# Optimization experiments

Measured on AMD Instinct MI355X. Metric: run time of the kernel, lower is better.

## Reference

```python
import math
import jax, jax.numpy as jnp
import numpy as np

D = 192      # d_model
NH = 8       # heads
NL = 2       # levels
NP = 4       # points
HD = D // NH # head dim = 24
GROUPS = 32


def layer_norm(x, g, b, eps=1e-5):
    mu = x.mean(-1, keepdims=True)
    var = ((x - mu) ** 2).mean(-1, keepdims=True)
    return (x - mu) / jnp.sqrt(var + eps) * g + b


def group_norm(x, g, b, eps=1e-5):
    # x: [B, C, H, W]
    B, C, H, W = x.shape
    xg = x.reshape(B, GROUPS, C // GROUPS, H, W)
    mu = xg.mean((2, 3, 4), keepdims=True)
    var = ((xg - mu) ** 2).mean((2, 3, 4), keepdims=True)
    xn = ((xg - mu) / jnp.sqrt(var + eps)).reshape(B, C, H, W)
    return xn * g[None, :, None, None] + b[None, :, None, None]


def pos_embed_2d(H, W):
    # PositionalEncoding2D(96, normalize=True) with an all-valid mask
    eps = 1e-6
    scale = 2 * math.pi
    npf = 96
    y = (jnp.arange(1, H + 1, dtype=jnp.float32) - 0.5) / (H + eps) * scale
    x = (jnp.arange(1, W + 1, dtype=jnp.float32) - 0.5) / (W + eps) * scale
    dim_t = 10000.0 ** (2.0 * (jnp.arange(npf) // 2).astype(jnp.float32) / npf)
    def enc(v):
        p = v[:, None] / dim_t  # [N, 96]
        return jnp.stack([jnp.sin(p[:, 0::2]), jnp.cos(p[:, 1::2])], -1).reshape(v.shape[0], npf)
    pe_y, pe_x = enc(y), enc(x)
    pos = jnp.concatenate([
        jnp.broadcast_to(pe_y[:, None, :], (H, W, npf)),
        jnp.broadcast_to(pe_x[None, :, :], (H, W, npf)),
    ], -1)  # [H, W, 192] (y-part first, like torch cat((pos_y, pos_x)))
    return pos.reshape(H * W, 2 * npf)


def ms_sample(value_h, loc, H, W):
    # value_h: [B, NH, H*W, HD]; loc: [B, NH, Lq, NP, 2] normalized to [0,1]
    # Replicates F.grid_sample(mode='bilinear', padding_mode='zeros', align_corners=False)
    B, _, Lq, P, _ = loc.shape
    x = loc[..., 0] * W - 0.5
    y = loc[..., 1] * H - 0.5
    x0 = jnp.floor(x)
    y0 = jnp.floor(y)
    wx = x - x0
    wy = y - y0
    def corner(xc, yc, w):
        valid = (xc >= 0) & (xc <= W - 1) & (yc >= 0) & (yc <= H - 1)
        xi = jnp.clip(xc, 0, W - 1).astype(jnp.int32)
        yi = jnp.clip(yc, 0, H - 1).astype(jnp.int32)
        idx = (yi * W + xi).reshape(B, NH, Lq * P)
        g = jnp.take_along_axis(value_h, idx[..., None], axis=2).reshape(B, NH, Lq, P, HD)
        return g * (w * valid)[..., None]
    return (corner(x0, y0, (1 - wx) * (1 - wy))
            + corner(x0 + 1, y0, wx * (1 - wy))
            + corner(x0, y0 + 1, (1 - wx) * wy)
            + corner(x0 + 1, y0 + 1, wx * wy))


def encoder_forward(src, pos, ref_pts, shapes, p):
    B, L, _ = src.shape
    starts = np.cumsum([0] + [h * w for h, w in shapes])
    offset_norm = jnp.array([[w, h] for h, w in shapes], jnp.float32)  # [NL, 2] = (W, H)
    out = src
    n_layers = p['so_W'].shape[0]
    for i in range(n_layers):
        q = out + pos
        off = (q @ p['so_W'][i] + p['so_b'][i]).reshape(B, L, NH, NL, NP, 2)
        aw = (q @ p['aw_W'][i] + p['aw_b'][i]).reshape(B, L, NH, NL * NP)
        aw = jax.nn.softmax(aw, -1).reshape(B, L, NH, NL, NP)
        loc = ref_pts[None, :, None, :, None, :] + off / offset_norm[None, None, None, :, None, :]
        v = (out @ p['vp_W'][i] + p['vp_b'][i]).reshape(B, L, NH, HD).transpose(0, 2, 1, 3)
        sampled = []
        for l, (h, w) in enumerate(shapes):
            vl = v[:, :, starts[l]:starts[l + 1], :]
            locl = loc[:, :, :, l].transpose(0, 2, 1, 3, 4)  # [B, NH, L, NP, 2]
            sampled.append(ms_sample(vl, locl, h, w))
        sampled = jnp.stack(sampled, 3)  # [B, NH, L, NL, NP, HD]
        awh = aw.transpose(0, 2, 1, 3, 4)  # [B, NH, L, NL, NP]
        attn = jnp.einsum('bhqlp,bhqlpc->bhqc', awh, sampled)
        attn = attn.transpose(0, 2, 1, 3).reshape(B, L, D)
        attn = attn @ p['op_W'][i] + p['op_b'][i]
        out = layer_norm(out + attn, p['ln1_g'][i], p['ln1_b'][i])
        ff = jax.nn.relu(out @ p['l1_W'][i] + p['l1_b'][i]) @ p['l2_W'][i] + p['l2_b'][i]
        out = layer_norm(out + ff, p['ln2_g'][i], p['ln2_b'][i])
    return out


def _feature_encoder(feat0, feat1, proj_w0, proj_b0, gn_g0, gn_b0,
                     proj_w1, proj_b1, gn_g1, gn_b1, level_embed, p):
    feats = [feat0, feat1]
    projs = [(proj_w0, proj_b0, gn_g0, gn_b0), (proj_w1, proj_b1, gn_g1, gn_b1)]
    shapes = [(int(f.shape[2]), int(f.shape[3])) for f in feats]
    B = feat0.shape[0]
    srcs, poss, refs = [], [], []
    for l, f in enumerate(feats):
        w, b, g, bb = projs[l]
        s = jnp.einsum('bchw,oc->bohw', f, w) + b[None, :, None, None]  # 1x1 conv
        s = group_norm(s, g, bb)
        srcs.append(s.reshape(B, D, -1).transpose(0, 2, 1))
        poss.append(pos_embed_2d(*shapes[l]) + level_embed[l])
        h, wdt = shapes[l]
        ry, rx = jnp.meshgrid(jnp.linspace(0.5, h - 0.5, h) / h,
                              jnp.linspace(0.5, wdt - 0.5, wdt) / wdt, indexing='ij')
        refs.append(jnp.stack([rx.reshape(-1), ry.reshape(-1)], -1))
    src = jnp.concatenate(srcs, 1)                # [B, Ltot, D]
    pos = jnp.concatenate(poss, 0)[None]          # [1, Ltot, D]
    # full-size images => masks all False => valid_ratios == 1
    ref_pts = jnp.broadcast_to(jnp.concatenate(refs, 0)[:, None, :], (src.shape[1], NL, 2))
    mem = encoder_forward(src, pos, ref_pts, shapes, p)
    n0 = shapes[0][0] * shapes[0][1]
    m0 = mem[:, :n0].reshape(B, shapes[0][0], shapes[0][1], D).transpose(0, 3, 1, 2)
    m1 = mem[:, n0:].reshape(B, shapes[1][0], shapes[1][1], D).transpose(0, 3, 1, 2)
    return m0, m1


def setup_inputs() -> dict:
    key = jax.random.key(0)
    ks = jax.random.split(key, 20)
    L = 6
    s = 0.02
    d = {}
    d['feat0'] = jax.random.normal(ks[0], (2, D, 96, 96), jnp.float32)
    d['feat1'] = jax.random.normal(ks[1], (2, D, 48, 48), jnp.float32)
    d['imgs'] = jax.random.normal(ks[2], (2, 3, 384, 384), jnp.float32)
    d['proj_w0'] = jax.random.normal(ks[3], (D, D), jnp.float32) * s
    d['proj_b0'] = jnp.zeros((D,), jnp.float32)
    d['gn_g0'] = jnp.ones((D,), jnp.float32)
    d['gn_b0'] = jnp.zeros((D,), jnp.float32)
    d['proj_w1'] = jax.random.normal(ks[4], (D, D), jnp.float32) * s
    d['proj_b1'] = jnp.zeros((D,), jnp.float32)
    d['gn_g1'] = jnp.ones((D,), jnp.float32)
    d['gn_b1'] = jnp.zeros((D,), jnp.float32)
    d['level_embed'] = jax.random.normal(ks[5], (NL, D), jnp.float32) * s
    d['so_W'] = jax.random.normal(ks[6], (L, D, NH * NL * NP * 2), jnp.float32) * s
    d['so_b'] = jax.random.normal(ks[7], (L, NH * NL * NP * 2), jnp.float32) * s
    d['aw_W'] = jax.random.normal(ks[8], (L, D, NH * NL * NP), jnp.float32) * s
    d['aw_b'] = jnp.zeros((L, NH * NL * NP), jnp.float32)
    d['vp_W'] = jax.random.normal(ks[9], (L, D, D), jnp.float32) * s
    d['vp_b'] = jnp.zeros((L, D), jnp.float32)
    d['op_W'] = jax.random.normal(ks[10], (L, D, D), jnp.float32) * s
    d['op_b'] = jnp.zeros((L, D), jnp.float32)
    d['ln1_g'] = jnp.ones((L, D), jnp.float32)
    d['ln1_b'] = jnp.zeros((L, D), jnp.float32)
    d['l1_W'] = jax.random.normal(ks[11], (L, D, 256), jnp.float32) * s
    d['l1_b'] = jnp.zeros((L, 256), jnp.float32)
    d['l2_W'] = jax.random.normal(ks[12], (L, 256, D), jnp.float32) * s
    d['l2_b'] = jnp.zeros((L, D), jnp.float32)
    d['ln2_g'] = jnp.ones((L, D), jnp.float32)
    d['ln2_b'] = jnp.zeros((L, D), jnp.float32)
    return d


def reference(feat0, feat1, imgs, proj_w0, proj_b0, gn_g0, gn_b0,
              proj_w1, proj_b1, gn_g1, gn_b1, level_embed,
              so_W, so_b, aw_W, aw_b, vp_W, vp_b, op_W, op_b,
              ln1_g, ln1_b, l1_W, l1_b, l2_W, l2_b, ln2_g, ln2_b):
    # imgs is only used for image sizes; full-size => all-valid masks
    p = dict(so_W=so_W, so_b=so_b, aw_W=aw_W, aw_b=aw_b, vp_W=vp_W, vp_b=vp_b,
             op_W=op_W, op_b=op_b, ln1_g=ln1_g, ln1_b=ln1_b,
             l1_W=l1_W, l1_b=l1_b, l2_W=l2_W, l2_b=l2_b, ln2_g=ln2_g, ln2_b=ln2_b)
    return _feature_encoder(feat0, feat1, proj_w0, proj_b0, gn_g0, gn_b0,
                            proj_w1, proj_b1, gn_g1, gn_b1, level_embed, p)
```

## Files before the change

kernel.cpp:

```cpp
#include <hip/hip_runtime.h>
#include <hip/hip_bf16.h>
#include <math.h>

#define Bb 2
#define Dm 192
#define NHh 8
#define HDd 24
#define N0 9216
#define N1 2304
#define LSEQ 11520
#define FFD 256
#define Mrows (Bb*LSEQ)

typedef __attribute__((ext_vector_type(8))) short short8;
typedef __attribute__((ext_vector_type(4))) float f32x4;

#define F_OUT 0
#define F_PRE (F_OUT + 4423680)
#define F_POS (F_PRE + 4423680)
#define F_LOC (F_POS + 2211840)
#define F_AW  (F_LOC + 2949120)
#define F_QB  (F_AW + 1474560)
#define F_OB  (F_QB + 2211840)
#define F_AH  (F_OB + 2211840)
#define F_WT16 (F_AH + 2949120)
#define F_BC  (F_WT16 + 626688)
#define F_GNS (F_BC + 1152)
#define F_V2  (F_GNS + 256)

#define WL_STRIDE 208896
#define WL_SOAW 0
#define WL_VP   36864
#define WL_OP   73728
#define WL_L1   110592
#define WL_L2   159744

__device__ inline __hip_bfloat16 f2b(float f) { return __float2bfloat16(f); }
__device__ inline unsigned short f2bu(float f) {
    __hip_bfloat16 h = __float2bfloat16(f);
    return *reinterpret_cast<unsigned short*>(&h);
}

__global__ void k_pos(float* pos, const float* level_embed) {
    int idx = blockIdx.x * 256 + threadIdx.x;
    if (idx >= LSEQ * Dm) return;
    int t = idx / Dm, d = idx % Dm;
    int lvl, row, col, H, W;
    if (t < N0) { lvl = 0; H = 96; W = 96; row = t / 96; col = t % 96; }
    else        { lvl = 1; H = 48; W = 48; int tl = t - N0; row = tl / 48; col = tl % 48; }
    int k = d % 96;
    float v;
    if (d < 96) v = (row + 0.5f) / ((float)H + 1e-6f) * 6.2831853071795864f;
    else        v = (col + 0.5f) / ((float)W + 1e-6f) * 6.2831853071795864f;
    float expo = (float)(k - (k & 1)) / 96.0f;
    float tm = exp2f(expo * 13.287712379549449f);
    float p = v / tm;
    float pe = (k & 1) ? cosf(p) : sinf(p);
    pos[idx] = pe + level_embed[lvl * Dm + d];
}

__global__ void k_prep(const float* soW, const float* awW, const float* vpW,
        const float* opW, const float* l1W, const float* l2W,
        const float* sob, const float* awb,
        __hip_bfloat16* WT, float* BC) {
    int idx = blockIdx.x * 256 + threadIdx.x;
    if (idx < 6 * 192) {
        int i = idx / 192, n = idx % 192;
        BC[idx] = (n < 128) ? sob[i * 128 + n] : awb[i * 64 + (n - 128)];
    }
    if (idx >= 6 * WL_STRIDE) return;
    int i = idx / WL_STRIDE; int r = idx % WL_STRIDE;
    float v;
    if (r < 36864)       { int n = r / 192, k = r % 192;
        v = (n < 128) ? soW[((size_t)i * 192 + k) * 128 + n]
                      : awW[((size_t)i * 192 + k) * 64 + (n - 128)]; }
    else if (r < 73728)  { int q = r - 36864;  int n = q / 192, k = q % 192;
        v = vpW[((size_t)i * 192 + k) * 192 + n]; }
    else if (r < 110592) { int q = r - 73728;  int n = q / 192, k = q % 192;
        v = opW[((size_t)i * 192 + k) * 192 + n]; }
    else if (r < 159744) { int q = r - 110592; int n = q / 192, k = q % 192;
        v = l1W[((size_t)i * 192 + k) * 256 + n]; }
    else                 { int q = r - 159744; int n = q / 256, k = q % 256;
        v = l2W[((size_t)i * 256 + k) * 192 + n]; }
    WT[idx] = f2b(v);
}

__global__ void k_prepc(const float* w0, const float* w1, __hip_bfloat16* cwb) {
    int idx = blockIdx.x * 256 + threadIdx.x;
    if (idx >= 2 * 36864) return;
    const float* w = (idx < 36864) ? w0 : w1;
    int r = idx % 36864;
    cwb[idx] = f2b(w[r]);
}

__global__ void k_tf(const float* feat, __hip_bfloat16* out, int HW, int st) {
    __shared__ float tile[32][33];
    int t0 = blockIdx.x * 32, c0 = blockIdx.y * 32, b = blockIdx.z;
    int tx = threadIdx.x, ty = threadIdx.y;
    #pragma unroll
    for (int k = 0; k < 4; k++) {
        int c = c0 + ty + k * 8;
        tile[ty + k * 8][tx] = feat[((size_t)b * Dm + c) * HW + t0 + tx];
    }
    __syncthreads();
    #pragma unroll
    for (int k = 0; k < 4; k++) {
        int t = t0 + ty + k * 8;
        out[((size_t)b * LSEQ + st + t) * Dm + c0 + tx] = f2b(tile[tx][ty + k * 8]);
    }
}

__global__ __launch_bounds__(192) void k_gnp(const float* __restrict__ pre,
        float* __restrict__ part) {
    int bid = blockIdx.x;
    int b = bid / 120; int r = bid % 120;
    int l = (r >= 96) ? 1 : 0; int ch = l ? (r - 96) : r;
    int start = b * LSEQ + (l ? N0 : 0) + ch * 96;
    int d = threadIdx.x;
    float s = 0.f, sq = 0.f;
    for (int t = 0; t < 96; t++) {
        float x = pre[(size_t)(start + t) * Dm + d];
        s += x; sq += x * x;
    }
    __shared__ float ls[192], lq[192];
    ls[d] = s; lq[d] = sq;
    __syncthreads();
    if (d < 32) {
        float a = 0.f, b2 = 0.f;
        #pragma unroll
        for (int j = 0; j < 6; j++) { a += ls[d * 6 + j]; b2 += lq[d * 6 + j]; }
        part[((size_t)bid * 32 + d) * 2]     = a;
        part[((size_t)bid * 32 + d) * 2 + 1] = b2;
    }
}

__global__ void k_gnf(const float* __restrict__ part, float* __restrict__ gns) {
    int bid = blockIdx.x;
    int b = bid >> 6; int l = (bid >> 5) & 1; int g = bid & 31;
    int nch = l ? 24 : 96;
    int base = b * 120 + (l ? 96 : 0);
    int tid = threadIdx.x;
    float s = 0.f, q = 0.f;
    for (int c = tid; c < nch; c += 64) {
        s += part[((size_t)(base + c) * 32 + g) * 2];
        q += part[((size_t)(base + c) * 32 + g) * 2 + 1];
    }
    for (int m = 1; m < 64; m <<= 1) { s += __shfl_xor(s, m, 64); q += __shfl_xor(q, m, 64); }
    if (tid == 0) {
        float total = (float)((l ? N1 : N0) * 6);
        float mean = s / total;
        float var = q / total - mean * mean;
        gns[bid * 2] = mean;
        gns[bid * 2 + 1] = rsqrtf(var + 1e-5f);
    }
}

__global__ void k_gnnorm(const float* srcp, const float* gns,
        const float* g0, const float* b0, const float* g1, const float* b1,
        const float* pos, float* out, __hip_bfloat16* ob, __hip_bfloat16* qb) {
    int idx = blockIdx.x * 256 + threadIdx.x;
    if (idx >= Bb * LSEQ * Dm) return;
    int d = idx % Dm;
    int t = (idx / Dm) % LSEQ;
    int l = (t < N0) ? 0 : 1;
    int g = d / 6;
    int b = idx / (Dm * LSEQ);
    int sid = ((b * 2 + l) * 32 + g) * 2;
    float mean = gns[sid], rstd = gns[sid + 1];
    float gg = l ? g1[d] : g0[d];
    float bbv = l ? b1[d] : b0[d];
    float v = (srcp[idx] - mean) * rstd * gg + bbv;
    out[idx] = v;
    ob[idx] = f2b(v);
    qb[idx] = f2b(v + pos[idx - (size_t)b * LSEQ * Dm]);
}

template<int KSTEPS>
__global__ __launch_bounds__(256) void k_gemm(
        const __hip_bfloat16* __restrict__ A,
        const __hip_bfloat16* __restrict__ Bt,
        const float* __restrict__ bias,
        float* __restrict__ Cf, int N) {
    constexpr int K = KSTEPS * 32;
    int wid = threadIdx.x >> 6, lane = threadIdx.x & 63;
    int lg = lane >> 4, lr = lane & 15;
    int row0 = blockIdx.x * 64 + wid * 16;
    int col0 = blockIdx.y * 64;
    const short* a_base = (const short*)A + (size_t)(row0 + lr) * K + lg * 8;
    const short* b_base = (const short*)Bt + (size_t)(col0 + lr) * K + lg * 8;
    f32x4 acc[4] = {};
    #pragma unroll
    for (int kk = 0; kk < KSTEPS; kk++) {
        short8 af = *(const short8*)(a_base + kk * 32);
        #pragma unroll
        for (int n = 0; n < 4; n++) {
            short8 bfr = *(const short8*)(b_base + (size_t)n * 16 * K + kk * 32);
            acc[n] = __builtin_amdgcn_mfma_f32_16x16x32_bf16(af, bfr, acc[n], 0, 0, 0);
        }
    }
    #pragma unroll
    for (int n = 0; n < 4; n++) {
        int col = col0 + n * 16 + lr;
        float bv = bias[col];
        #pragma unroll
        for (int r = 0; r < 4; r++) {
            int row = row0 + lg * 4 + r;
            Cf[(size_t)row * N + col] = acc[n][r] + bv;
        }
    }
}

__global__ __launch_bounds__(192) void k_soawvp(
        const __hip_bfloat16* __restrict__ QB,
        const __hip_bfloat16* __restrict__ OB,
        const __hip_bfloat16* __restrict__ BtS,
        const __hip_bfloat16* __restrict__ BtV,
        const float* __restrict__ biasS,
        const float* __restrict__ biasV,
        float* __restrict__ LOC, float* __restrict__ AW,
        float* __restrict__ VF) {
    constexpr int K = 192;
    int wid = threadIdx.x >> 6, lane = threadIdx.x & 63;
    int lg = lane >> 4, lr = lane & 15;
    int row0 = blockIdx.x * 32;
    int col0 = wid * 64;
    int role = blockIdx.y;
    const short* A  = (const short*)(role ? OB : QB);
    const short* Bt = (const short*)(role ? BtV : BtS);
    const float* bias = role ? biasV : biasS;
    short8 bw[24];
    {
        const short* b_base = Bt + (size_t)(col0 + lr) * K + lg * 8;
        #pragma unroll
        for (int n = 0; n < 4; n++)
            #pragma unroll
            for (int kk = 0; kk < 6; kk++)
                bw[n * 6 + kk] = *(const short8*)(b_base + (size_t)n * 16 * K + kk * 32);
    }
    #pragma unroll
    for (int rg = 0; rg < 2; rg++) {
        const short* a_base = A + (size_t)(row0 + rg * 16 + lr) * K + lg * 8;
        f32x4 acc[4] = {};
        #pragma unroll
        for (int kk = 0; kk < 6; kk++) {
            short8 af = *(const short8*)(a_base + kk * 32);
            #pragma unroll
            for (int n = 0; n < 4; n++)
                acc[n] = __builtin_amdgcn_mfma_f32_16x16x32_bf16(af, bw[n * 6 + kk], acc[n], 0, 0, 0);
        }
        #pragma unroll
        for (int n = 0; n < 4; n++) {
            float bv = bias[col0 + n * 16 + lr];
            #pragma unroll
            for (int r = 0; r < 4; r++) acc[n][r] += bv;
        }
        int rbase = row0 + rg * 16;
        if (role) {
            #pragma unroll
            for (int n = 0; n < 4; n++) {
                int col = col0 + n * 16 + lr;
                #pragma unroll
                for (int r = 0; r < 4; r++)
                    VF[(size_t)(rbase + lg * 4 + r) * Dm + col] = acc[n][r];
            }
        } else if (wid == 2) {
            #pragma unroll
            for (int n = 0; n < 4; n++) {
                #pragma unroll
                for (int r = 0; r < 4; r++) {
                    float v = acc[n][r];
                    float m = v;
                    m = fmaxf(m, __shfl_xor(m, 1)); m = fmaxf(m, __shfl_xor(m, 2));
                    m = fmaxf(m, __shfl_xor(m, 4));
                    float e = expf(v - m);
                    float sm = e;
                    sm += __shfl_xor(sm, 1); sm += __shfl_xor(sm, 2); sm += __shfl_xor(sm, 4);
                    AW[(size_t)(rbase + lg * 4 + r) * 64 + n * 16 + lr] = e / sm;
                }
            }
        } else {
            #pragma unroll
            for (int r = 0; r < 4; r++) {
                int row = rbase + lg * 4 + r;
                int t = (row >= LSEQ) ? row - LSEQ : row;
                int rr, cc, Ht, Wt;
                if (t < N0) { Ht = 96; Wt = 96; rr = t / 96; cc = t % 96; }
                else        { Ht = 48; Wt = 48; int tl = t - N0; rr = tl / 48; cc = tl % 48; }
                float refx = (cc + 0.5f) / (float)Wt;
                float refy = (rr + 0.5f) / (float)Ht;
                #pragma unroll
                for (int n = 0; n < 4; n++) {
                    int col = col0 + n * 16 + lr;
                    int j = col >> 1, comp = col & 1;
                    float sc = (j & 4) ? 48.f : 96.f;
                    LOC[(size_t)row * 128 + col] = (comp ? refy : refx) + acc[n][r] / sc;
                }
            }
        }
    }
}

template<bool LAST>
__global__ __launch_bounds__(256) void k_tail(
        const float* __restrict__ Vin,
        float* __restrict__ LOC, float* __restrict__ AW,
        const __hip_bfloat16* __restrict__ BtOp, const float* __restrict__ bOp,
        const __hip_bfloat16* __restrict__ Bt1, const float* __restrict__ b1,
        const __hip_bfloat16* __restrict__ Bt2, const float* __restrict__ b2,
        const float* __restrict__ g1, const float* __restrict__ t1,
        const float* __restrict__ g2, const float* __restrict__ t2,
        const float* __restrict__ pos,
        float* __restrict__ OUTp,
        const __hip_bfloat16* __restrict__ BtS,
        const __hip_bfloat16* __restrict__ BtV,
        const float* __restrict__ biasS, const float* __restrict__ biasV,
        float* __restrict__ Vout) {
    __shared__ __align__(16) short ybf[32][200];
    __shared__ __align__(16) short hid[32][264];
    __shared__ float aw_s[32][64];
    __shared__ float ps[4][32], pq[4][32];
    int tid = threadIdx.x;
    int wid = tid >> 6, lane = tid & 63, lg = lane >> 4, lr = lane & 15;
    int row0 = blockIdx.x * 32;
    float yres[2][3][4];
    {
        float* loc_s = (float*)&hid[0][0];
        for (int idx = tid; idx < 32 * 128; idx += 256)
            loc_s[idx] = LOC[(size_t)row0 * 128 + idx];
        for (int idx = tid; idx < 32 * 64; idx += 256)
            aw_s[idx >> 6][idx & 63] = AW[(size_t)row0 * 64 + idx];
        __syncthreads();
        for (int tt6 = 0; tt6 < 6; tt6++) {
            int id = tid + tt6 * 256;
            int tl = id / 48;
            int l48 = id - tl * 48;
            int h = l48 / 6, dq = l48 - h * 6;
            int row = row0 + tl;
            int bb = (row >= LSEQ) ? 1 : 0;
            const float* vbase = Vin + (size_t)bb * LSEQ * Dm + h * HDd + dq * 4;
            float a0 = 0.f, a1 = 0.f, a2 = 0.f, a3 = 0.f;
            #pragma unroll
            for (int lp = 0; lp < 8; lp++) {
                int l = lp >> 2;
                int Wl = l ? 48 : 96, Hl = l ? 48 : 96, st = l ? N0 : 0;
                float a  = aw_s[tl][h * 8 + lp];
                float lx = loc_s[tl * 128 + (h * 8 + lp) * 2];
                float ly = loc_s[tl * 128 + (h * 8 + lp) * 2 + 1];
                float x = lx * (float)Wl - 0.5f, y = ly * (float)Hl - 0.5f;
                float x0f = floorf(x), y0f = floorf(y);
                float wx = x - x0f, wy = y - y0f;
                int x0 = (int)x0f, y0 = (int)y0f;
                #pragma unroll
                for (int cy = 0; cy < 2; cy++) {
                    int yi = y0 + cy;
                    float wyv = cy ? wy : 1.f - wy;
                    bool vy = (yi >= 0) && (yi < Hl);
                    int yc = min(max(yi, 0), Hl - 1);
                    #pragma unroll
                    for (int cx = 0; cx < 2; cx++) {
                        int xi = x0 + cx;
                        float wv = (cx ? wx : 1.f - wx) * wyv;
                        bool ok = vy && (xi >= 0) && (xi < Wl);
                        int xc = min(max(xi, 0), Wl - 1);
                        float cw = ok ? a * wv : 0.f;
                        float4 g4 = *(const float4*)(vbase + (size_t)(st + yc * Wl + xc) * Dm);
                        a0 += cw * g4.x; a1 += cw * g4.y;
                        a2 += cw * g4.z; a3 += cw * g4.w;
                    }
                }
            }
            ushort4 o4;
            o4.x = f2bu(a0); o4.y = f2bu(a1); o4.z = f2bu(a2); o4.w = f2bu(a3);
            *(ushort4*)&ybf[tl][h * HDd + dq * 4] = o4;
        }
        __syncthreads();
    }
    {
        float resid[2][3][4];
        #pragma unroll
        for (int rg = 0; rg < 2; rg++)
            #pragma unroll
            for (int n = 0; n < 3; n++) {
                int col = wid * 48 + n * 16 + lr;
                #pragma unroll
                for (int r = 0; r < 4; r++)
                    resid[rg][n][r] = OUTp[(size_t)(row0 + rg * 16 + lg * 4 + r) * Dm + col];
            }
        const short* b_base = (const short*)BtOp + (size_t)(wid * 48 + lr) * 192 + lg * 8;
        f32x4 acc[2][3] = {};
        #pragma unroll
        for (int kk = 0; kk < 6; kk++) {
            short8 af0 = *(const short8*)&ybf[lr][lg * 8 + kk * 32];
            short8 af1 = *(const short8*)&ybf[16 + lr][lg * 8 + kk * 32];
            #pragma unroll
            for (int n = 0; n < 3; n++) {
                short8 bfr = *(const short8*)(b_base + (size_t)n * 16 * 192 + kk * 32);
                acc[0][n] = __builtin_amdgcn_mfma_f32_16x16x32_bf16(af0, bfr, acc[0][n], 0, 0, 0);
                acc[1][n] = __builtin_amdgcn_mfma_f32_16x16x32_bf16(af1, bfr, acc[1][n], 0, 0, 0);
            }
        }
        #pragma unroll
        for (int rg = 0; rg < 2; rg++) {
            float s[4] = {0.f, 0.f, 0.f, 0.f}, q[4] = {0.f, 0.f, 0.f, 0.f};
            #pragma unroll
            for (int n = 0; n < 3; n++) {
                int col = wid * 48 + n * 16 + lr;
                float bv = bOp[col];
                #pragma unroll
                for (int r = 0; r < 4; r++) {
                    float v = acc[rg][n][r] + bv + resid[rg][n][r];
                    acc[rg][n][r] = v;
                    s[r] += v; q[r] += v * v;
                }
            }
            #pragma unroll
            for (int r = 0; r < 4; r++) {
                #pragma unroll
                for (int m = 1; m < 16; m <<= 1) {
                    s[r] += __shfl_xor(s[r], m); q[r] += __shfl_xor(q[r], m);
                }
            }
            if (lr == 0) {
                #pragma unroll
                for (int r = 0; r < 4; r++) {
                    ps[wid][rg * 16 + lg * 4 + r] = s[r];
                    pq[wid][rg * 16 + lg * 4 + r] = q[r];
                }
            }
        }
        __syncthreads();
        #pragma unroll
        for (int rg = 0; rg < 2; rg++) {
            float mean[4], rstd[4];
            #pragma unroll
            for (int r = 0; r < 4; r++) {
                int rl = rg * 16 + lg * 4 + r;
                float S = ps[0][rl] + ps[1][rl] + ps[2][rl] + ps[3][rl];
                float Q = pq[0][rl] + pq[1][rl] + pq[2][rl] + pq[3][rl];
                mean[r] = S * (1.f / Dm);
                float var = Q * (1.f / Dm) - mean[r] * mean[r];
                rstd[r] = rsqrtf(var + 1e-5f);
            }
            #pragma unroll
            for (int n = 0; n < 3; n++) {
                int col = wid * 48 + n * 16 + lr;
                float gg = g1[col], bb = t1[col];
                #pragma unroll
                for (int r = 0; r < 4; r++) {
                    float y = (acc[rg][n][r] - mean[r]) * rstd[r] * gg + bb;
                    yres[rg][n][r] = y;
                    ybf[rg * 16 + lg * 4 + r][col] = (short)f2bu(y);
                }
            }
        }
        __syncthreads();
    }
    {
        const short* b_base = (const short*)Bt1 + (size_t)(wid * 64 + lr) * 192 + lg * 8;
        f32x4 acc[2][4] = {};
        #pragma unroll
        for (int kk = 0; kk < 6; kk++) {
            short8 af0 = *(const short8*)&ybf[lr][lg * 8 + kk * 32];
            short8 af1 = *(const short8*)&ybf[16 + lr][lg * 8 + kk * 32];
            #pragma unroll
            for (int n = 0; n < 4; n++) {
                short8 bfr = *(const short8*)(b_base + (size_t)n * 16 * 192 + kk * 32);
                acc[0][n] = __builtin_amdgcn_mfma_f32_16x16x32_bf16(af0, bfr, acc[0][n], 0, 0, 0);
                acc[1][n] = __builtin_amdgcn_mfma_f32_16x16x32_bf16(af1, bfr, acc[1][n], 0, 0, 0);
            }
        }
        #pragma unroll
        for (int rg = 0; rg < 2; rg++)
            #pragma unroll
            for (int n = 0; n < 4; n++) {
                int col = wid * 64 + n * 16 + lr;
                float bv = b1[col];
                #pragma unroll
                for (int r = 0; r < 4; r++)
                    hid[rg * 16 + lg * 4 + r][col] = (short)f2bu(fmaxf(acc[rg][n][r] + bv, 0.f));
            }
        __syncthreads();
    }
    {
        const short* b_base = (const short*)Bt2 + (size_t)(wid * 48 + lr) * 256 + lg * 8;
        f32x4 acc[2][3] = {};
        #pragma unroll
        for (int kk = 0; kk < 8; kk++) {
            short8 af0 = *(const short8*)&hid[lr][lg * 8 + kk * 32];
            short8 af1 = *(const short8*)&hid[16 + lr][lg * 8 + kk * 32];
            #pragma unroll
            for (int n = 0; n < 3; n++) {
                short8 bfr = *(const short8*)(b_base + (size_t)n * 16 * 256 + kk * 32);
                acc[0][n] = __builtin_amdgcn_mfma_f32_16x16x32_bf16(af0, bfr, acc[0][n], 0, 0, 0);
                acc[1][n] = __builtin_amdgcn_mfma_f32_16x16x32_bf16(af1, bfr, acc[1][n], 0, 0, 0);
            }
        }
        #pragma unroll
        for (int rg = 0; rg < 2; rg++) {
            float s[4] = {0.f, 0.f, 0.f, 0.f}, q[4] = {0.f, 0.f, 0.f, 0.f};
            #pragma unroll
            for (int n = 0; n < 3; n++) {
                int col = wid * 48 + n * 16 + lr;
                float bv = b2[col];
                #pragma unroll
                for (int r = 0; r < 4; r++) {
                    float v = acc[rg][n][r] + bv + yres[rg][n][r];
                    acc[rg][n][r] = v;
                    s[r] += v; q[r] += v * v;
                }
            }
            #pragma unroll
            for (int r = 0; r < 4; r++) {
                #pragma unroll
                for (int m = 1; m < 16; m <<= 1) {
                    s[r] += __shfl_xor(s[r], m); q[r] += __shfl_xor(q[r], m);
                }
            }
            if (lr == 0) {
                #pragma unroll
                for (int r = 0; r < 4; r++) {
                    ps[wid][rg * 16 + lg * 4 + r] = s[r];
                    pq[wid][rg * 16 + lg * 4 + r] = q[r];
                }
            }
        }
        __syncthreads();
        #pragma unroll
        for (int rg = 0; rg < 2; rg++) {
            float mean[4], rstd[4];
            #pragma unroll
            for (int r = 0; r < 4; r++) {
                int rl = rg * 16 + lg * 4 + r;
                float S = ps[0][rl] + ps[1][rl] + ps[2][rl] + ps[3][rl];
                float Q = pq[0][rl] + pq[1][rl] + pq[2][rl] + pq[3][rl];
                mean[r] = S * (1.f / Dm);
                float var = Q * (1.f / Dm) - mean[r] * mean[r];
                rstd[r] = rsqrtf(var + 1e-5f);
            }
            #pragma unroll
            for (int n = 0; n < 3; n++) {
                int col = wid * 48 + n * 16 + lr;
                float gg = g2[col], bb = t2[col];
                #pragma unroll
                for (int r = 0; r < 4; r++) {
                    int row = row0 + rg * 16 + lg * 4 + r;
                    int rl = rg * 16 + lg * 4 + r;
                    float y = (acc[rg][n][r] - mean[r]) * rstd[r] * gg + bb;
                    OUTp[(size_t)row * Dm + col] = y;
                    if (!LAST) {
                        ybf[rl][col] = (short)f2bu(y);
                        int tp = (row >= LSEQ) ? row - LSEQ : row;
                        hid[rl][col] = (short)f2bu(y + pos[(size_t)tp * Dm + col]);
                    }
                }
            }
        }
    }
    if (LAST) return;
    __syncthreads();
    {
        const short* b_base = (const short*)BtV + (size_t)(wid * 48 + lr) * 192 + lg * 8;
        f32x4 acc[2][3] = {};
        #pragma unroll
        for (int kk = 0; kk < 6; kk++) {
            short8 af0 = *(const short8*)&ybf[lr][lg * 8 + kk * 32];
            short8 af1 = *(const short8*)&ybf[16 + lr][lg * 8 + kk * 32];
            #pragma unroll
            for (int n = 0; n < 3; n++) {
                short8 bfr = *(const short8*)(b_base + (size_t)n * 16 * 192 + kk * 32);
                acc[0][n] = __builtin_amdgcn_mfma_f32_16x16x32_bf16(af0, bfr, acc[0][n], 0, 0, 0);
                acc[1][n] = __builtin_amdgcn_mfma_f32_16x16x32_bf16(af1, bfr, acc[1][n], 0, 0, 0);
            }
        }
        #pragma unroll
        for (int rg = 0; rg < 2; rg++)
            #pragma unroll
            for (int n = 0; n < 3; n++) {
                int col = wid * 48 + n * 16 + lr;
                float bv = biasV[col];
                #pragma unroll
                for (int r = 0; r < 4; r++)
                    Vout[(size_t)(row0 + rg * 16 + lg * 4 + r) * Dm + col] = acc[rg][n][r] + bv;
            }
    }
    {
        const short* b_base = (const short*)BtS + (size_t)(wid * 48 + lr) * 192 + lg * 8;
        f32x4 acc[2][3] = {};
        #pragma unroll
        for (int kk = 0; kk < 6; kk++) {
            short8 af0 = *(const short8*)&hid[lr][lg * 8 + kk * 32];
            short8 af1 = *(const short8*)&hid[16 + lr][lg * 8 + kk * 32];
            #pragma unroll
            for (int n = 0; n < 3; n++) {
                short8 bfr = *(const short8*)(b_base + (size_t)n * 16 * 192 + kk * 32);
                acc[0][n] = __builtin_amdgcn_mfma_f32_16x16x32_bf16(af0, bfr, acc[0][n], 0, 0, 0);
                acc[1][n] = __builtin_amdgcn_mfma_f32_16x16x32_bf16(af1, bfr, acc[1][n], 0, 0, 0);
            }
        }
        #pragma unroll
        for (int rg = 0; rg < 2; rg++) {
            #pragma unroll
            for (int n = 0; n < 3; n++) {
                int col = wid * 48 + n * 16 + lr;
                float bv = biasS[col];
                if (col >= 128) {
                    #pragma unroll
                    for (int r = 0; r < 4; r++) {
                        float v = acc[rg][n][r] + bv;
                        float m = v;
                        m = fmaxf(m, __shfl_xor(m, 1)); m = fmaxf(m, __shfl_xor(m, 2));
                        m = fmaxf(m, __shfl_xor(m, 4));
                        float e = expf(v - m);
                        float sm = e;
                        sm += __shfl_xor(sm, 1); sm += __shfl_xor(sm, 2); sm += __shfl_xor(sm, 4);
                        AW[(size_t)(row0 + rg * 16 + lg * 4 + r) * 64 + (col - 128)] = e / sm;
                    }
                } else {
                    #pragma unroll
                    for (int r = 0; r < 4; r++) {
                        int row = row0 + rg * 16 + lg * 4 + r;
                        int t = (row >= LSEQ) ? row - LSEQ : row;
                        int rr, cc, Ht, Wt;
                        if (t < N0) { Ht = 96; Wt = 96; rr = t / 96; cc = t % 96; }
                        else        { Ht = 48; Wt = 48; int tl = t - N0; rr = tl / 48; cc = tl % 48; }
                        float refx = (cc + 0.5f) / (float)Wt;
                        float refy = (rr + 0.5f) / (float)Ht;
                        int j = col >> 1;
                        float sc = (j & 4) ? 48.f : 96.f;
                        LOC[(size_t)row * 128 + col] =
                            ((col & 1) ? refy : refx) + (acc[rg][n][r] + bv) / sc;
                    }
                }
            }
        }
    }
}

__global__ void k_outt(const float* __restrict__ out, float* __restrict__ dst,
        int HW, int st) {
    __shared__ float tile[32][33];
    int t0 = blockIdx.x * 32, d0 = blockIdx.y * 32, b = blockIdx.z;
    int tx = threadIdx.x, ty = threadIdx.y;
    #pragma unroll
    for (int k = 0; k < 4; k++) {
        int t = t0 + ty + k * 8;
        tile[ty + k * 8][tx] = out[((size_t)b * LSEQ + st + t) * Dm + d0 + tx];
    }
    __syncthreads();
    #pragma unroll
    for (int k = 0; k < 4; k++) {
        int d = d0 + ty + k * 8;
        dst[((size_t)b * Dm + d) * HW + t0 + tx] = tile[tx][ty + k * 8];
    }
}

extern "C" void kernel_launch(void* const* d_in, const int* in_sizes, int n_in,
                              void* d_out, int out_size, void* d_ws, size_t ws_size,
                              hipStream_t stream) {
    (void)in_sizes; (void)n_in; (void)out_size; (void)ws_size;
    const float* feat0   = (const float*)d_in[0];
    const float* feat1   = (const float*)d_in[1];
    const float* proj_w0 = (const float*)d_in[3];
    const float* proj_b0 = (const float*)d_in[4];
    const float* gn_g0   = (const float*)d_in[5];
    const float* gn_b0   = (const float*)d_in[6];
    const float* proj_w1 = (const float*)d_in[7];
    const float* proj_b1 = (const float*)d_in[8];
    const float* gn_g1   = (const float*)d_in[9];
    const float* gn_b1   = (const float*)d_in[10];
    const float* level_embed = (const float*)d_in[11];
    const float* so_W = (const float*)d_in[12];
    const float* so_b = (const float*)d_in[13];
    const float* aw_W = (const float*)d_in[14];
    const float* aw_b = (const float*)d_in[15];
    const float* vp_W = (const float*)d_in[16];
    const float* vp_b = (const float*)d_in[17];
    const float* op_W = (const float*)d_in[18];
    const float* op_b = (const float*)d_in[19];
    const float* ln1_g = (const float*)d_in[20];
    const float* ln1_b = (const float*)d_in[21];
    const float* l1_W = (const float*)d_in[22];
    const float* l1_b = (const float*)d_in[23];
    const float* l2_W = (const float*)d_in[24];
    const float* l2_b = (const float*)d_in[25];
    const float* ln2_g = (const float*)d_in[26];
    const float* ln2_b = (const float*)d_in[27];

    float* ws   = (float*)d_ws;
    float* OUT  = ws + F_OUT;
    float* PRE  = ws + F_PRE;
    float* POS  = ws + F_POS;
    float* LOC  = ws + F_LOC;
    float* AWp  = ws + F_AW;
    float* V2   = ws + F_V2;
    __hip_bfloat16* QB  = (__hip_bfloat16*)(ws + F_QB);
    __hip_bfloat16* OB  = (__hip_bfloat16*)(ws + F_OB);
    __hip_bfloat16* WT16 = (__hip_bfloat16*)(ws + F_WT16);
    float* BC   = ws + F_BC;
    float* GNS  = ws + F_GNS;
    __hip_bfloat16* FEATB = (__hip_bfloat16*)(ws + F_LOC);
    __hip_bfloat16* CWB   = (__hip_bfloat16*)(ws + F_AW);
    float* GPART = ws + F_AH;

    k_pos<<<(LSEQ * Dm + 255) / 256, 256, 0, stream>>>(POS, level_embed);
    k_prep<<<(6 * WL_STRIDE + 255) / 256, 256, 0, stream>>>(so_W, aw_W, vp_W, op_W,
        l1_W, l2_W, so_b, aw_b, WT16, BC);
    k_prepc<<<(2 * 36864 + 255) / 256, 256, 0, stream>>>(proj_w0, proj_w1, CWB);
    k_tf<<<dim3(N0 / 32, 6, 2), dim3(32, 8), 0, stream>>>(feat0, FEATB, N0, 0);
    k_tf<<<dim3(N1 / 32, 6, 2), dim3(32, 8), 0, stream>>>(feat1, FEATB, N1, N0);
    for (int b = 0; b < 2; b++) {
        k_gemm<6><<<dim3(N0 / 64, 3), 256, 0, stream>>>(
            FEATB + (size_t)b * LSEQ * Dm, CWB, proj_b0,
            PRE + (size_t)b * LSEQ * Dm, Dm);
        k_gemm<6><<<dim3(N1 / 64, 3), 256, 0, stream>>>(
            FEATB + ((size_t)b * LSEQ + N0) * Dm, CWB + 36864, proj_b1,
            PRE + ((size_t)b * LSEQ + N0) * Dm, Dm);
    }
    k_gnp<<<240, 192, 0, stream>>>(PRE, GPART);
    k_gnf<<<128, 64, 0, stream>>>(GPART, GNS);
    k_gnnorm<<<(Bb * LSEQ * Dm + 255) / 256, 256, 0, stream>>>(PRE, GNS,
        gn_g0, gn_b0, gn_g1, gn_b1, POS, OUT, OB, QB);

    k_soawvp<<<dim3(Mrows / 32, 2), 192, 0, stream>>>(
        QB, OB, WT16 + WL_SOAW, WT16 + WL_VP, BC, vp_b, LOC, AWp, V2);

    float* Vin = V2;
    float* Vout = PRE;
    for (int i = 0; i < 6; i++) {
        const __hip_bfloat16* WL = WT16 + (size_t)i * WL_STRIDE;
        if (i < 5) {
            const __hip_bfloat16* WN = WT16 + (size_t)(i + 1) * WL_STRIDE;
            k_tail<false><<<Mrows / 32, 256, 0, stream>>>(
                Vin, LOC, AWp,
                WL + WL_OP, op_b + (size_t)i * Dm,
                WL + WL_L1, l1_b + (size_t)i * FFD,
                WL + WL_L2, l2_b + (size_t)i * Dm,
                ln1_g + (size_t)i * Dm, ln1_b + (size_t)i * Dm,
                ln2_g + (size_t)i * Dm, ln2_b + (size_t)i * Dm, POS, OUT,
                WN + WL_SOAW, WN + WL_VP, BC + (i + 1) * 192,
                vp_b + (size_t)(i + 1) * Dm, Vout);
        } else {
            k_tail<true><<<Mrows / 32, 256, 0, stream>>>(
                Vin, LOC, AWp,
                WL + WL_OP, op_b + (size_t)i * Dm,
                WL + WL_L1, l1_b + (size_t)i * FFD,
                WL + WL_L2, l2_b + (size_t)i * Dm,
                ln1_g + (size_t)i * Dm, ln1_b + (size_t)i * Dm,
                ln2_g + (size_t)i * Dm, ln2_b + (size_t)i * Dm, POS, OUT,
                nullptr, nullptr, nullptr, nullptr, nullptr);
        }
        float* tswap = Vin; Vin = Vout; Vout = tswap;
    }
    k_outt<<<dim3(N0 / 32, 6, 2), dim3(32, 8), 0, stream>>>(OUT, (float*)d_out, N0, 0);
    k_outt<<<dim3(N1 / 32, 6, 2), dim3(32, 8), 0, stream>>>(OUT,
        (float*)d_out + (size_t)Bb * Dm * N0, N1, N0);
}
```

Baseline: 642.5 us.

## Split deformable sampling out of fused tail kernel into separate kernel

Moves the bilinear multi-scale sampling from the start of each k_tail block into a new k_sample kernel with small 192-thread blocks covering 4 tokens each. The sampled attention output is written as bf16 to a workspace buffer, and k_tail loads its MFMA A fragments straight from global memory instead of shared memory. The aim is more parallelism and better latency hiding for the gather-heavy sampling, which was bound to the larger fused blocks. The cost is an extra launch per layer and a global round trip of the attention activations.

```diff
diff --git a/kernel.cpp b/kernel.cpp
--- a/kernel.cpp
+++ b/kernel.cpp
@@ -300,9 +300,62 @@
     }
 }
 
+__global__ __launch_bounds__(192) void k_sample(const float* __restrict__ V,
+        const float* __restrict__ LOC, const float* __restrict__ AW,
+        __hip_bfloat16* __restrict__ ATT) {
+    __shared__ float aw_s[4][64];
+    __shared__ float loc_s[4][128];
+    int tid = threadIdx.x;
+    int tg0 = blockIdx.x * 4;
+    for (int idx = tid; idx < 256; idx += 192)
+        aw_s[idx >> 6][idx & 63] = AW[(size_t)tg0 * 64 + idx];
+    for (int idx = tid; idx < 512; idx += 192)
+        loc_s[idx >> 7][idx & 127] = LOC[(size_t)tg0 * 128 + idx];
+    __syncthreads();
+    int tt = tid / 48, lane = tid - tt * 48;
+    int h = lane / 6, dq = lane - h * 6;
+    int tg = tg0 + tt;
+    int b = (tg >= LSEQ) ? 1 : 0;
+    const float* vb = V + (size_t)b * LSEQ * Dm + h * HDd + dq * 4;
+    float a0 = 0.f, a1 = 0.f, a2 = 0.f, a3 = 0.f;
+    #pragma unroll
+    for (int lp = 0; lp < 8; lp++) {
+        int l = lp >> 2;
+        int Wl = l ? 48 : 96, Hl = l ? 48 : 96, st = l ? N0 : 0;
+        float a  = aw_s[tt][h * 8 + lp];
+        float lx = loc_s[tt][(h * 8 + lp) * 2];
+        float ly = loc_s[tt][(h * 8 + lp) * 2 + 1];
+        float x = lx * (float)Wl - 0.5f, y = ly * (float)Hl - 0.5f;
+        float x0f = floorf(x), y0f = floorf(y);
+        float wx = x - x0f, wy = y - y0f;
+        int x0 = (int)x0f, y0 = (int)y0f;
+        #pragma unroll
+        for (int cy = 0; cy < 2; cy++) {
+            int yi = y0 + cy;
+            float wyv = cy ? wy : 1.f - wy;
+            bool vy = (yi >= 0) && (yi < Hl);
+            int yc = min(max(yi, 0), Hl - 1);
+            #pragma unroll
+            for (int cx = 0; cx < 2; cx++) {
+                int xi = x0 + cx;
+                float wv = (cx ? wx : 1.f - wx) * wyv;
+                bool ok = vy && (xi >= 0) && (xi < Wl);
+                int xc = min(max(xi, 0), Wl - 1);
+                float cw = ok ? a * wv : 0.f;
+                float4 g4 = *(const float4*)(vb + (size_t)(st + yc * Wl + xc) * Dm);
+                a0 += cw * g4.x; a1 += cw * g4.y;
+                a2 += cw * g4.z; a3 += cw * g4.w;
+            }
+        }
+    }
+    ushort4 o4;
+    o4.x = f2bu(a0); o4.y = f2bu(a1); o4.z = f2bu(a2); o4.w = f2bu(a3);
+    *(ushort4*)((unsigned short*)ATT + (size_t)tg * Dm + h * HDd + dq * 4) = o4;
+}
+
 template<bool LAST>
 __global__ __launch_bounds__(256) void k_tail(
-        const float* __restrict__ Vin,
+        const __hip_bfloat16* __restrict__ ATT,
         float* __restrict__ LOC, float* __restrict__ AW,
         const __hip_bfloat16* __restrict__ BtOp, const float* __restrict__ bOp,
         const __hip_bfloat16* __restrict__ Bt1, const float* __restrict__ b1,
@@ -317,65 +370,12 @@
         float* __restrict__ Vout) {
     __shared__ __align__(16) short ybf[32][200];
     __shared__ __align__(16) short hid[32][264];
-    __shared__ float aw_s[32][64];
     __shared__ float ps[4][32], pq[4][32];
     int tid = threadIdx.x;
     int wid = tid >> 6, lane = tid & 63, lg = lane >> 4, lr = lane & 15;
     int row0 = blockIdx.x * 32;
     float yres[2][3][4];
     {
-        float* loc_s = (float*)&hid[0][0];
-        for (int idx = tid; idx < 32 * 128; idx += 256)
-            loc_s[idx] = LOC[(size_t)row0 * 128 + idx];
-        for (int idx = tid; idx < 32 * 64; idx += 256)
-            aw_s[idx >> 6][idx & 63] = AW[(size_t)row0 * 64 + idx];
-        __syncthreads();
-        for (int tt6 = 0; tt6 < 6; tt6++) {
-            int id = tid + tt6 * 256;
-            int tl = id / 48;
-            int l48 = id - tl * 48;
-            int h = l48 / 6, dq = l48 - h * 6;
-            int row = row0 + tl;
-            int bb = (row >= LSEQ) ? 1 : 0;
-            const float* vbase = Vin + (size_t)bb * LSEQ * Dm + h * HDd + dq * 4;
-            float a0 = 0.f, a1 = 0.f, a2 = 0.f, a3 = 0.f;
-            #pragma unroll
-            for (int lp = 0; lp < 8; lp++) {
-                int l = lp >> 2;
-                int Wl = l ? 48 : 96, Hl = l ? 48 : 96, st = l ? N0 : 0;
-                float a  = aw_s[tl][h * 8 + lp];
-                float lx = loc_s[tl * 128 + (h * 8 + lp) * 2];
-                float ly = loc_s[tl * 128 + (h * 8 + lp) * 2 + 1];
-                float x = lx * (float)Wl - 0.5f, y = ly * (float)Hl - 0.5f;
-                float x0f = floorf(x), y0f = floorf(y);
-                float wx = x - x0f, wy = y - y0f;
-                int x0 = (int)x0f, y0 = (int)y0f;
-                #pragma unroll
-                for (int cy = 0; cy < 2; cy++) {
-                    int yi = y0 + cy;
-                    float wyv = cy ? wy : 1.f - wy;
-                    bool vy = (yi >= 0) && (yi < Hl);
-                    int yc = min(max(yi, 0), Hl - 1);
-                    #pragma unroll
-                    for (int cx = 0; cx < 2; cx++) {
-                        int xi = x0 + cx;
-                        float wv = (cx ? wx : 1.f - wx) * wyv;
-                        bool ok = vy && (xi >= 0) && (xi < Wl);
-                        int xc = min(max(xi, 0), Wl - 1);
-                        float cw = ok ? a * wv : 0.f;
-                        float4 g4 = *(const float4*)(vbase + (size_t)(st + yc * Wl + xc) * Dm);
-                        a0 += cw * g4.x; a1 += cw * g4.y;
-                        a2 += cw * g4.z; a3 += cw * g4.w;
-                    }
-                }
-            }
-            ushort4 o4;
-            o4.x = f2bu(a0); o4.y = f2bu(a1); o4.z = f2bu(a2); o4.w = f2bu(a3);
-            *(ushort4*)&ybf[tl][h * HDd + dq * 4] = o4;
-        }
-        __syncthreads();
-    }
-    {
         float resid[2][3][4];
         #pragma unroll
         for (int rg = 0; rg < 2; rg++)
@@ -386,12 +386,14 @@
                 for (int r = 0; r < 4; r++)
                     resid[rg][n][r] = OUTp[(size_t)(row0 + rg * 16 + lg * 4 + r) * Dm + col];
             }
+        const short* a0 = (const short*)ATT + (size_t)(row0 + lr) * 192 + lg * 8;
+        const short* a1 = (const short*)ATT + (size_t)(row0 + 16 + lr) * 192 + lg * 8;
         const short* b_base = (const short*)BtOp + (size_t)(wid * 48 + lr) * 192 + lg * 8;
         f32x4 acc[2][3] = {};
         #pragma unroll
         for (int kk = 0; kk < 6; kk++) {
-            short8 af0 = *(const short8*)&ybf[lr][lg * 8 + kk * 32];
-            short8 af1 = *(const short8*)&ybf[16 + lr][lg * 8 + kk * 32];
+            short8 af0 = *(const short8*)(a0 + kk * 32);
+            short8 af1 = *(const short8*)(a1 + kk * 32);
             #pragma unroll
             for (int n = 0; n < 3; n++) {
                 short8 bfr = *(const short8*)(b_base + (size_t)n * 16 * 192 + kk * 32);
@@ -695,6 +697,7 @@
     float* V2   = ws + F_V2;
     __hip_bfloat16* QB  = (__hip_bfloat16*)(ws + F_QB);
     __hip_bfloat16* OB  = (__hip_bfloat16*)(ws + F_OB);
+    __hip_bfloat16* AH  = (__hip_bfloat16*)(ws + F_AH);
     __hip_bfloat16* WT16 = (__hip_bfloat16*)(ws + F_WT16);
     float* BC   = ws + F_BC;
     float* GNS  = ws + F_GNS;
@@ -728,10 +731,11 @@
     float* Vout = PRE;
     for (int i = 0; i < 6; i++) {
         const __hip_bfloat16* WL = WT16 + (size_t)i * WL_STRIDE;
+        k_sample<<<Mrows / 4, 192, 0, stream>>>(Vin, LOC, AWp, AH);
         if (i < 5) {
             const __hip_bfloat16* WN = WT16 + (size_t)(i + 1) * WL_STRIDE;
             k_tail<false><<<Mrows / 32, 256, 0, stream>>>(
-                Vin, LOC, AWp,
+                AH, LOC, AWp,
                 WL + WL_OP, op_b + (size_t)i * Dm,
                 WL + WL_L1, l1_b + (size_t)i * FFD,
                 WL + WL_L2, l2_b + (size_t)i * Dm,
@@ -741,7 +745,7 @@
                 vp_b + (size_t)(i + 1) * Dm, Vout);
         } else {
             k_tail<true><<<Mrows / 32, 256, 0, stream>>>(
-                Vin, LOC, AWp,
+                AH, LOC, AWp,
                 WL + WL_OP, op_b + (size_t)i * Dm,
                 WL + WL_L1, l1_b + (size_t)i * FFD,
                 WL + WL_L2, l2_b + (size_t)i * Dm,
```

Result: no change. 645.3 us (+0.4%).
